# Optimization experiments

Hardware: AMD Instinct MI355X
Metric: run time of the kernel (lower is better)

The kernel has to match this reference:

```python
import jax, jax.numpy as jnp
import numpy as np

COV_LOSS_WT = 1.0


def setup_inputs() -> dict:
    key = jax.random.key(0)
    ks = jax.random.split(key, 6)
    B, T, S, H = 8, 64, 256, 768
    sc = 1.0 / np.sqrt(H)
    return {
        "decoder_outputs": jax.random.normal(ks[0], (B, T, H), jnp.float32),
        "decoder_input_mask": jnp.ones((B, T), jnp.float32),
        "encoder_outputs": jax.random.normal(ks[1], (B, S, H), jnp.float32),
        "enc_padding_mask": jnp.ones((B, S), jnp.float32),
        "coverage": jnp.zeros((B, S), jnp.float32),
        "W_h": (jax.random.normal(ks[2], (H, H), jnp.float32) * sc),
        "W_dec": (jax.random.normal(ks[3], (H, H), jnp.float32) * sc),
        "b_dec": jnp.zeros((H,), jnp.float32),
        "w_c": (jax.random.normal(ks[4], (H,), jnp.float32) * sc),
        "v": (jax.random.normal(ks[5], (H,), jnp.float32) * sc),
    }


def reference(decoder_outputs, decoder_input_mask, encoder_outputs,
              enc_padding_mask, coverage, W_h, W_dec, b_dec, w_c, v):
    # Precompute projections (same math as expanding att_features then adding
    # the coverage feature per step).
    enc_feature = encoder_outputs @ W_h.T                 # [B,S,H]
    dec_fea = decoder_outputs @ W_dec.T + b_dec           # [B,T,H]

    def step(cov, dec_t):
        # cov: [B,S], dec_t: [B,H]
        e = jnp.tanh(enc_feature + dec_t[:, None, :] + cov[:, :, None] * w_c)  # [B,S,H]
        scores = e @ v                                    # [B,S]
        attn = jax.nn.softmax(scores, axis=-1) * enc_padding_mask
        attn = attn / attn.sum(-1, keepdims=True)
        ht = jnp.einsum('bs,bsh->bh', attn, encoder_outputs)
        step_loss = COV_LOSS_WT * jnp.sum(jnp.minimum(attn, cov), axis=-1)     # [B]
        return cov + attn, (ht, attn, step_loss)

    coverage_final, (ht, attn, step_losses) = jax.lax.scan(
        step, coverage, jnp.swapaxes(dec_fea, 0, 1))      # scan over T

    ht_hat = jnp.swapaxes(ht, 0, 1)                       # [B,T,H]
    attn_dist = jnp.swapaxes(attn, 0, 1)                  # [B,T,S]
    converge_loss = jnp.sum(step_losses * decoder_input_mask.T) / jnp.sum(decoder_input_mask)
    return (ht_hat, attn_dist, converge_loss, coverage_final)
```

## Files before the change

### kernel.cpp

```cpp
#include <hip/hip_runtime.h>

#define Bq 8
#define Tq 64
#define Sq 256
#define Hq 768
#define TT 8
#define ST 16

typedef float f32x4 __attribute__((ext_vector_type(4)));
typedef __bf16 bf16x8 __attribute__((ext_vector_type(8)));

#define TANH_SCALE 2.885390081777927f
#define LOG2E 1.4426950408889634f

template <int Ctrl, int Rmask>
__device__ __forceinline__ float dpp_add_f(float v) {
  int t = __builtin_amdgcn_update_dpp(0, __float_as_int(v), Ctrl, Rmask, 0xF, true);
  return v + __int_as_float(t);
}
__device__ __forceinline__ float wave64_sum(float v) {
  v = dpp_add_f<0xB1, 0xF>(v);
  v = dpp_add_f<0x4E, 0xF>(v);
  v = dpp_add_f<0x141, 0xF>(v);
  v = dpp_add_f<0x140, 0xF>(v);
  v = dpp_add_f<0x142, 0xA>(v);
  v = dpp_add_f<0x143, 0xC>(v);
  return __int_as_float(__builtin_amdgcn_readlane(__float_as_int(v), 63));
}

__device__ __forceinline__ uint2 cvt4(f32x4 v) {
  union { __bf16 h[4]; uint2 u; } t;
  t.h[0] = (__bf16)v[0]; t.h[1] = (__bf16)v[1];
  t.h[2] = (__bf16)v[2]; t.h[3] = (__bf16)v[3];
  return t.u;
}

__global__ __launch_bounds__(256, 4) void proj_kernel(
    const float* __restrict__ enc, const float* __restrict__ dec,
    const float* __restrict__ Wh, const float* __restrict__ Wd,
    const float* __restrict__ bd,
    const float* __restrict__ wcvec, const float* __restrict__ vvec,
    __bf16* __restrict__ efh, __bf16* __restrict__ decfh,
    float* __restrict__ w1g, float* __restrict__ lacc)
{
  {
    int gidx = blockIdx.x * 256 + threadIdx.x;
    if (gidx < Hq) w1g[gidx] = vvec[gidx] * wcvec[gidx];
    if (gidx == 0) lacc[0] = 0.f;
  }

  __shared__ unsigned short As[2][32][40];
  __shared__ unsigned short Bs[2][64][40];

  int bid = blockIdx.x;
  const float* A; const float* W; bool isEf;
  int bm, bn;
  if (bid < 768) {
    A = enc; W = Wh; isEf = true;
    bm = bid % 64; bn = bid / 64;
  } else {
    bid -= 768;
    A = dec; W = Wd; isEf = false;
    bm = bid % 16; bn = bid / 16;
  }
  const int m0 = bm * 32, n0 = bn * 64;

  const int ti = threadIdx.x;
  const int rowA = ti >> 3, colA = (ti & 7) * 4;
  const int rowB = ti >> 2, colB = (ti & 3) * 8;
  const float* pa = A + (size_t)(m0 + rowA) * Hq + colA;
  const float* pw = W + (size_t)(n0 + rowB) * Hq + colB;

  {
    f32x4 a0 = *(const f32x4*)pa;
    f32x4 w0 = *(const f32x4*)pw, w1 = *(const f32x4*)(pw + 4);
    *(uint2*)&As[0][rowA][colA]     = cvt4(a0);
    *(uint2*)&Bs[0][rowB][colB]     = cvt4(w0);
    *(uint2*)&Bs[0][rowB][colB + 4] = cvt4(w1);
  }
  __syncthreads();

  const int w = ti >> 6, ln = ti & 63;
  const int mh = (w >> 1) * 16, nh = (w & 1) * 32;
  const int rsel = ln & 15, kofe = (ln >> 4) * 8;

  f32x4 acc[2] = {};
  for (int k = 0; k < 24; k++) {
    f32x4 na, nw0, nw1;
    if (k < 23) {
      na  = *(const f32x4*)(pa + (k + 1) * 32);
      nw0 = *(const f32x4*)(pw + (k + 1) * 32);
      nw1 = *(const f32x4*)(pw + (k + 1) * 32 + 4);
    }
    const int cur = k & 1;
    bf16x8 af = *(const bf16x8*)&As[cur][mh + rsel][kofe];
    bf16x8 b0 = *(const bf16x8*)&Bs[cur][nh + rsel][kofe];
    bf16x8 b1 = *(const bf16x8*)&Bs[cur][nh + 16 + rsel][kofe];
    acc[0] = __builtin_amdgcn_mfma_f32_16x16x32_bf16(af, b0, acc[0], 0, 0, 0);
    acc[1] = __builtin_amdgcn_mfma_f32_16x16x32_bf16(af, b1, acc[1], 0, 0, 0);
    if (k < 23) {
      const int nxt = cur ^ 1;
      *(uint2*)&As[nxt][rowA][colA]     = cvt4(na);
      *(uint2*)&Bs[nxt][rowB][colB]     = cvt4(nw0);
      *(uint2*)&Bs[nxt][rowB][colB + 4] = cvt4(nw1);
      __syncthreads();
    }
  }

  const int col = ln & 15, rb = (ln >> 4) * 4;
#pragma unroll
  for (int tn = 0; tn < 2; tn++)
#pragma unroll
    for (int j = 0; j < 4; j++) {
      int r = m0 + mh + rb + j, c = n0 + nh + tn * 16 + col;
      float val = acc[tn][j];
      if (isEf) {
        efh[(size_t)r * Hq + c] =
            (__bf16)__builtin_amdgcn_exp2f(val * TANH_SCALE);
      } else {
        decfh[(size_t)r * Hq + c] =
            (__bf16)__builtin_amdgcn_exp2f((val + bd[c]) * TANH_SCALE);
      }
    }
}

__global__ __launch_bounds__(256, 4) void abcd_kernel(
    const __bf16* __restrict__ efh, const __bf16* __restrict__ decfh,
    const float* __restrict__ vvec, const float* __restrict__ w1g,
    float2* __restrict__ ab)
{
  __shared__ unsigned short efs[ST][780];
  __shared__ unsigned short dts[TT][776];
  __shared__ float part[128][2];
  const int b = blockIdx.x & 7;
  const int r = blockIdx.x >> 3;
  const int tt0 = (r & 7) * TT;
  const int st0 = (r >> 3) * ST;
  const int tid = threadIdx.x;

  for (int i = tid; i < ST * 192; i += 256) {
    int row = i / 192, c = (i % 192) * 4;
    *(uint2*)&efs[row][c] =
        *(const uint2*)(efh + (size_t)(b * Sq + st0 + row) * Hq + c);
  }
  for (int i = tid; i < TT * 192; i += 256) {
    int row = i / 192, c = (i % 192) * 4;
    *(uint2*)&dts[row][c] =
        *(const uint2*)(decfh + (size_t)(b * Tq + tt0 + row) * Hq + c);
  }
  __syncthreads();

  const int hh = tid >> 7;
  const int pid = tid & 127;
  const int tl = pid >> 4, sl = pid & 15;
  const int hbase = hh * 384;
  const int hbu = __builtin_amdgcn_readfirstlane(hbase);
  const float* vp  = vvec + hbu;
  const float* w1p = w1g + hbu;

  float A = 0.f, B = 0.f;
#define BLO(x) __uint_as_float((x) << 16)
#define BHI(x) __uint_as_float((x) & 0xFFFF0000u)
#pragma unroll 4
  for (int j = 0; j < 384; j += 4) {
    uint2 eu = *(const uint2*)&efs[sl][hbase + j];
    uint2 du = *(const uint2*)&dts[tl][hbase + j];
    f32x4 v4 = *(const f32x4*)(vp + j);
    f32x4 w1 = *(const f32x4*)(w1p + j);
    float e2[4];
    e2[0] = BLO(eu.x) * BLO(du.x);
    e2[1] = BHI(eu.x) * BHI(du.x);
    e2[2] = BLO(eu.y) * BLO(du.y);
    e2[3] = BHI(eu.y) * BHI(du.y);
#pragma unroll
    for (int e = 0; e < 4; e++) {
      float rr = __builtin_amdgcn_rcpf(1.f + e2[e]);
      float t0 = 1.f - 2.f * rr;
      float f1 = 1.f - t0 * t0;
      A += v4[e] * t0;
      B += w1[e] * f1;
    }
  }
#undef BLO
#undef BHI

  if (hh == 1) { part[pid][0] = A; part[pid][1] = B; }
  __syncthreads();
  if (hh == 0) {
    float2 outv;
    outv.x = A + part[pid][0];
    outv.y = B + part[pid][1];
    ab[(size_t)(b * Tq + tt0 + tl) * Sq + st0 + sl] = outv;
  }
}

__global__ __launch_bounds__(256, 1) void scan2_kernel(
    const float2* __restrict__ ab, const float* __restrict__ emask,
    const float* __restrict__ cov0, const float* __restrict__ dmask,
    float* __restrict__ out_attn, float* __restrict__ out_covf,
    float* __restrict__ lacc)
{
  __shared__ float zp[2][4];
  __shared__ float dms[Tq];
  __shared__ float lred[4];
  const int b = blockIdx.x;
  const int s = threadIdx.x;
  const int w = s >> 6, ln = s & 63;
  if (s < Tq) dms[s] = dmask[b * Tq + s];
  const float em = emask[b * Sq + s];
  float cov = cov0[b * Sq + s];
  float lp = 0.f;
  const float2* P = ab + (size_t)b * Tq * Sq + s;
  float2 cur = P[0];
  __syncthreads();

  for (int t = 0; t < Tq; t++) {
    float2 nxt = (t + 1 < Tq) ? P[(size_t)(t + 1) * Sq] : cur;
    float sc = cur.x + cov * cur.y;
    float E = __builtin_amdgcn_exp2f(sc * LOG2E) * em;
    float wsum = wave64_sum(E);
    if (ln == 0) zp[t & 1][w] = wsum;
    __syncthreads();
    float Z = zp[t & 1][0] + zp[t & 1][1] + zp[t & 1][2] + zp[t & 1][3];
    float at = E * __builtin_amdgcn_rcpf(Z);
    lp += fminf(at, cov) * dms[t];
    cov += at;
    out_attn[(size_t)(b * Tq + t) * Sq + s] = at;
    cur = nxt;
  }

  out_covf[b * Sq + s] = cov;
  float wl = wave64_sum(lp);
  if (ln == 0) lred[w] = wl;
  __syncthreads();
  if (s == 0) atomicAdd(lacc, lred[0] + lred[1] + lred[2] + lred[3]);
}

__global__ __launch_bounds__(256) void ht_kernel(
    const float* __restrict__ attn, const float* __restrict__ enc,
    const float* __restrict__ dmask, const float* __restrict__ lacc,
    float* __restrict__ out_ht, float* __restrict__ out_loss)
{
  __shared__ float lat[Sq][8];
  __shared__ float r4[4];
  int bid = blockIdx.x;
  int b = bid / 24, r = bid % 24, tc = r / 3, hc = r % 3;
  int tid = threadIdx.x;
  int h = hc * 256 + tid;
#pragma unroll
  for (int tt = 0; tt < 8; tt++)
    lat[tid][tt] = attn[(size_t)(b * Tq + tc * 8 + tt) * Sq + tid];
  __syncthreads();

  float acc[8] = {};
  const float* ep = enc + (size_t)(b * Sq) * Hq + h;
  for (int sb = 0; sb < Sq; sb += 8) {
    float e[8];
#pragma unroll
    for (int u = 0; u < 8; u++) e[u] = ep[(size_t)(sb + u) * Hq];
#pragma unroll
    for (int u = 0; u < 8; u++) {
      f32x4 a0 = *(const f32x4*)&lat[sb + u][0];
      f32x4 a1 = *(const f32x4*)&lat[sb + u][4];
      acc[0] += a0[0] * e[u]; acc[1] += a0[1] * e[u];
      acc[2] += a0[2] * e[u]; acc[3] += a0[3] * e[u];
      acc[4] += a1[0] * e[u]; acc[5] += a1[1] * e[u];
      acc[6] += a1[2] * e[u]; acc[7] += a1[3] * e[u];
    }
  }
#pragma unroll
  for (int tt = 0; tt < 8; tt++)
    out_ht[(size_t)(b * Tq + tc * 8 + tt) * Hq + h] = acc[tt];

  if (blockIdx.x == 0) {
    float s = 0.f;
    for (int i = tid; i < Bq * Tq; i += 256) s += dmask[i];
#pragma unroll
    for (int off = 32; off; off >>= 1) s += __shfl_xor(s, off);
    int w = tid >> 6, ln = tid & 63;
    if (ln == 0) r4[w] = s;
    __syncthreads();
    if (tid == 0) out_loss[0] = lacc[0] / (r4[0] + r4[1] + r4[2] + r4[3]);
  }
}

extern "C" void kernel_launch(void* const* d_in, const int* in_sizes, int n_in,
                              void* d_out, int out_size, void* d_ws, size_t ws_size,
                              hipStream_t stream) {
  const float* dec   = (const float*)d_in[0];
  const float* dmask = (const float*)d_in[1];
  const float* enc   = (const float*)d_in[2];
  const float* emask = (const float*)d_in[3];
  const float* cov0  = (const float*)d_in[4];
  const float* Wh    = (const float*)d_in[5];
  const float* Wd    = (const float*)d_in[6];
  const float* bd    = (const float*)d_in[7];
  const float* wc    = (const float*)d_in[8];
  const float* vv    = (const float*)d_in[9];
  float* out = (float*)d_out;

  char* ws = (char*)d_ws;
  __bf16* efh   = (__bf16*)ws;
  __bf16* decfh = (__bf16*)(ws + 3145728);
  float2* ab    = (float2*)(ws + 3932160);
  float*  w1g   = (float*)(ws + 4980736);
  float*  lacc  = (float*)(ws + 4983808);

  const size_t OFF_ATTN = (size_t)Bq * Tq * Hq;
  const size_t OFF_LOSS = OFF_ATTN + (size_t)Bq * Tq * Sq;
  const size_t OFF_COV  = OFF_LOSS + 1;

  proj_kernel<<<960, 256, 0, stream>>>(enc, dec, Wh, Wd, bd, wc, vv,
                                       efh, decfh, w1g, lacc);
  abcd_kernel<<<1024, 256, 0, stream>>>(efh, decfh, vv, w1g, ab);
  scan2_kernel<<<Bq, 256, 0, stream>>>(ab, emask, cov0, dmask,
                                       out + OFF_ATTN, out + OFF_COV, lacc);
  ht_kernel<<<192, 256, 0, stream>>>(out + OFF_ATTN, enc, dmask, lacc,
                                     out, out + OFF_LOSS);
}
```

Baseline: 90.92 us.

## Fuse score computation and coverage scan with per-chunk counters for overlap

Merges the score-producing kernel and the sequential softmax/coverage scan into one launch. The 8 scan blocks take the highest block indices and spin on per-(batch, time-chunk) atomic counters, so they can start on early time chunks while the remaining score blocks are still running. This removes a kernel launch boundary and overlaps the serial scan with producer work. The risk is deadlock or slowdown if the scan blocks get scheduled before producers, since the scan blocks occupy CUs while polling. It also relies on relaxed atomics with no acquire/release ordering between the ab stores and the counter.

```diff
diff --git a/kernel.cpp b/kernel.cpp
--- a/kernel.cpp
+++ b/kernel.cpp
@@ -41,11 +41,13 @@
     const float* __restrict__ bd,
     const float* __restrict__ wcvec, const float* __restrict__ vvec,
     __bf16* __restrict__ efh, __bf16* __restrict__ decfh,
-    float* __restrict__ w1g, float* __restrict__ lacc)
+    float* __restrict__ w1g, float* __restrict__ lacc,
+    unsigned* __restrict__ cnt)
 {
   {
     int gidx = blockIdx.x * 256 + threadIdx.x;
     if (gidx < Hq) w1g[gidx] = vvec[gidx] * wcvec[gidx];
+    if (gidx < 64) cnt[gidx] = 0u;
     if (gidx == 0) lacc[0] = 0.f;
   }
 
@@ -124,116 +126,138 @@
     }
 }
 
-__global__ __launch_bounds__(256, 4) void abcd_kernel(
+__global__ __launch_bounds__(256, 4) void abscan_kernel(
     const __bf16* __restrict__ efh, const __bf16* __restrict__ decfh,
     const float* __restrict__ vvec, const float* __restrict__ w1g,
-    float2* __restrict__ ab)
+    const float* __restrict__ emask, const float* __restrict__ cov0,
+    const float* __restrict__ dmask,
+    float2* __restrict__ ab,
+    float* __restrict__ out_attn, float* __restrict__ out_covf,
+    float* __restrict__ lacc, unsigned* __restrict__ cnt)
 {
-  __shared__ unsigned short efs[ST][780];
-  __shared__ unsigned short dts[TT][776];
-  __shared__ float part[128][2];
-  const int b = blockIdx.x & 7;
-  const int r = blockIdx.x >> 3;
-  const int tt0 = (r & 7) * TT;
-  const int st0 = (r >> 3) * ST;
+  __shared__ double smem_raw[4808];
+  const int bid = blockIdx.x;
   const int tid = threadIdx.x;
 
-  for (int i = tid; i < ST * 192; i += 256) {
-    int row = i / 192, c = (i % 192) * 4;
-    *(uint2*)&efs[row][c] =
-        *(const uint2*)(efh + (size_t)(b * Sq + st0 + row) * Hq + c);
-  }
-  for (int i = tid; i < TT * 192; i += 256) {
-    int row = i / 192, c = (i % 192) * 4;
-    *(uint2*)&dts[row][c] =
-        *(const uint2*)(decfh + (size_t)(b * Tq + tt0 + row) * Hq + c);
-  }
-  __syncthreads();
-
-  const int hh = tid >> 7;
-  const int pid = tid & 127;
-  const int tl = pid >> 4, sl = pid & 15;
-  const int hbase = hh * 384;
-  const int hbu = __builtin_amdgcn_readfirstlane(hbase);
-  const float* vp  = vvec + hbu;
-  const float* w1p = w1g + hbu;
-
-  float A = 0.f, B = 0.f;
+  if (bid < 1024) {
+    unsigned short (*efs)[780] = (unsigned short(*)[780])smem_raw;
+    unsigned short (*dts)[776] = (unsigned short(*)[776])((char*)smem_raw + 24960);
+    float (*part)[2]           = (float(*)[2])((char*)smem_raw + 37376);
+    const int b = bid & 7;
+    const int r = bid >> 3;
+    const int kchunk = r & 7;
+    const int tt0 = kchunk * TT;
+    const int st0 = (r >> 3) * ST;
+
+    for (int i = tid; i < ST * 192; i += 256) {
+      int row = i / 192, c = (i % 192) * 4;
+      *(uint2*)&efs[row][c] =
+          *(const uint2*)(efh + (size_t)(b * Sq + st0 + row) * Hq + c);
+    }
+    for (int i = tid; i < TT * 192; i += 256) {
+      int row = i / 192, c = (i % 192) * 4;
+      *(uint2*)&dts[row][c] =
+          *(const uint2*)(decfh + (size_t)(b * Tq + tt0 + row) * Hq + c);
+    }
+    __syncthreads();
+
+    const int hh = tid >> 7;
+    const int pid = tid & 127;
+    const int tl = pid >> 4, sl = pid & 15;
+    const int hbase = hh * 384;
+    const int hbu = __builtin_amdgcn_readfirstlane(hbase);
+    const float* vp  = vvec + hbu;
+    const float* w1p = w1g + hbu;
+
+    float A = 0.f, B = 0.f;
 #define BLO(x) __uint_as_float((x) << 16)
 #define BHI(x) __uint_as_float((x) & 0xFFFF0000u)
 #pragma unroll 4
-  for (int j = 0; j < 384; j += 4) {
-    uint2 eu = *(const uint2*)&efs[sl][hbase + j];
-    uint2 du = *(const uint2*)&dts[tl][hbase + j];
-    f32x4 v4 = *(const f32x4*)(vp + j);
-    f32x4 w1 = *(const f32x4*)(w1p + j);
-    float e2[4];
-    e2[0] = BLO(eu.x) * BLO(du.x);
-    e2[1] = BHI(eu.x) * BHI(du.x);
-    e2[2] = BLO(eu.y) * BLO(du.y);
-    e2[3] = BHI(eu.y) * BHI(du.y);
-#pragma unroll
-    for (int e = 0; e < 4; e++) {
-      float rr = __builtin_amdgcn_rcpf(1.f + e2[e]);
-      float t0 = 1.f - 2.f * rr;
-      float f1 = 1.f - t0 * t0;
-      A += v4[e] * t0;
-      B += w1[e] * f1;
-    }
-  }
+    for (int j = 0; j < 384; j += 4) {
+      uint2 eu = *(const uint2*)&efs[sl][hbase + j];
+      uint2 du = *(const uint2*)&dts[tl][hbase + j];
+      f32x4 v4 = *(const f32x4*)(vp + j);
+      f32x4 w1 = *(const f32x4*)(w1p + j);
+      float e2[4];
+      e2[0] = BLO(eu.x) * BLO(du.x);
+      e2[1] = BHI(eu.x) * BHI(du.x);
+      e2[2] = BLO(eu.y) * BLO(du.y);
+      e2[3] = BHI(eu.y) * BHI(du.y);
+#pragma unroll
+      for (int e = 0; e < 4; e++) {
+        float rr = __builtin_amdgcn_rcpf(1.f + e2[e]);
+        float t0 = 1.f - 2.f * rr;
+        float f1 = 1.f - t0 * t0;
+        A += v4[e] * t0;
+        B += w1[e] * f1;
+      }
+    }
 #undef BLO
 #undef BHI
 
-  if (hh == 1) { part[pid][0] = A; part[pid][1] = B; }
-  __syncthreads();
-  if (hh == 0) {
-    float2 outv;
-    outv.x = A + part[pid][0];
-    outv.y = B + part[pid][1];
-    ab[(size_t)(b * Tq + tt0 + tl) * Sq + st0 + sl] = outv;
-  }
-}
-
-__global__ __launch_bounds__(256, 1) void scan2_kernel(
-    const float2* __restrict__ ab, const float* __restrict__ emask,
-    const float* __restrict__ cov0, const float* __restrict__ dmask,
-    float* __restrict__ out_attn, float* __restrict__ out_covf,
-    float* __restrict__ lacc)
-{
-  __shared__ float zp[2][4];
-  __shared__ float dms[Tq];
-  __shared__ float lred[4];
-  const int b = blockIdx.x;
-  const int s = threadIdx.x;
-  const int w = s >> 6, ln = s & 63;
-  if (s < Tq) dms[s] = dmask[b * Tq + s];
-  const float em = emask[b * Sq + s];
-  float cov = cov0[b * Sq + s];
-  float lp = 0.f;
-  const float2* P = ab + (size_t)b * Tq * Sq + s;
-  float2 cur = P[0];
-  __syncthreads();
-
-  for (int t = 0; t < Tq; t++) {
-    float2 nxt = (t + 1 < Tq) ? P[(size_t)(t + 1) * Sq] : cur;
-    float sc = cur.x + cov * cur.y;
-    float E = __builtin_amdgcn_exp2f(sc * LOG2E) * em;
-    float wsum = wave64_sum(E);
-    if (ln == 0) zp[t & 1][w] = wsum;
-    __syncthreads();
-    float Z = zp[t & 1][0] + zp[t & 1][1] + zp[t & 1][2] + zp[t & 1][3];
-    float at = E * __builtin_amdgcn_rcpf(Z);
-    lp += fminf(at, cov) * dms[t];
-    cov += at;
-    out_attn[(size_t)(b * Tq + t) * Sq + s] = at;
-    cur = nxt;
-  }
-
-  out_covf[b * Sq + s] = cov;
-  float wl = wave64_sum(lp);
-  if (ln == 0) lred[w] = wl;
-  __syncthreads();
-  if (s == 0) atomicAdd(lacc, lred[0] + lred[1] + lred[2] + lred[3]);
+    if (hh == 1) { part[pid][0] = A; part[pid][1] = B; }
+    __syncthreads();
+    if (hh == 0) {
+      union { float2 f; unsigned long long u; } cv;
+      cv.f.x = A + part[pid][0];
+      cv.f.y = B + part[pid][1];
+      __hip_atomic_store(
+          (unsigned long long*)&ab[(size_t)(b * Tq + tt0 + tl) * Sq + st0 + sl],
+          cv.u, __ATOMIC_RELAXED, __HIP_MEMORY_SCOPE_AGENT);
+    }
+    __syncthreads();
+    if (tid == 0)
+      __hip_atomic_fetch_add(&cnt[b * 8 + kchunk], 1u,
+                             __ATOMIC_RELAXED, __HIP_MEMORY_SCOPE_AGENT);
+  } else {
+    float* zp   = (float*)smem_raw;
+    float* dms  = (float*)smem_raw + 8;
+    float* lred = (float*)smem_raw + 72;
+    const int b = bid - 1024;
+    const int s = tid, w = tid >> 6, ln = tid & 63;
+    if (tid < Tq) dms[tid] = dmask[b * Tq + tid];
+    const float em = emask[b * Sq + s];
+    float cov = cov0[b * Sq + s];
+    float lp = 0.f;
+    const unsigned long long* P =
+        (const unsigned long long*)(ab + (size_t)b * Tq * Sq + s);
+
+    for (int kc = 0; kc < 8; kc++) {
+      if (tid == 0)
+        while (__hip_atomic_load(&cnt[b * 8 + kc],
+                                 __ATOMIC_RELAXED, __HIP_MEMORY_SCOPE_AGENT) < 16u)
+          __builtin_amdgcn_s_sleep(2);
+      __syncthreads();
+
+      union { unsigned long long u; float2 f; } cv[8];
+#pragma unroll
+      for (int j = 0; j < 8; j++)
+        cv[j].u = __hip_atomic_load(P + (size_t)(kc * 8 + j) * Sq,
+                                    __ATOMIC_RELAXED, __HIP_MEMORY_SCOPE_AGENT);
+
+#pragma unroll
+      for (int j = 0; j < 8; j++) {
+        const int t = kc * 8 + j;
+        float sc = cv[j].f.x + cov * cv[j].f.y;
+        float E = __builtin_amdgcn_exp2f(sc * LOG2E) * em;
+        float wsum = wave64_sum(E);
+        if (ln == 0) zp[(t & 1) * 4 + w] = wsum;
+        __syncthreads();
+        float Z = zp[(t & 1) * 4 + 0] + zp[(t & 1) * 4 + 1] +
+                  zp[(t & 1) * 4 + 2] + zp[(t & 1) * 4 + 3];
+        float at = E * __builtin_amdgcn_rcpf(Z);
+        lp += fminf(at, cov) * dms[t];
+        cov += at;
+        out_attn[(size_t)(b * Tq + t) * Sq + s] = at;
+      }
+    }
+
+    out_covf[b * Sq + s] = cov;
+    float wl = wave64_sum(lp);
+    if (ln == 0) lred[w] = wl;
+    __syncthreads();
+    if (tid == 0) atomicAdd(lacc, lred[0] + lred[1] + lred[2] + lred[3]);
+  }
 }
 
 __global__ __launch_bounds__(256) void ht_kernel(
@@ -300,21 +324,23 @@
   float* out = (float*)d_out;
 
   char* ws = (char*)d_ws;
-  __bf16* efh   = (__bf16*)ws;
-  __bf16* decfh = (__bf16*)(ws + 3145728);
-  float2* ab    = (float2*)(ws + 3932160);
-  float*  w1g   = (float*)(ws + 4980736);
-  float*  lacc  = (float*)(ws + 4983808);
+  __bf16*   efh   = (__bf16*)ws;
+  __bf16*   decfh = (__bf16*)(ws + 3145728);
+  float2*   ab    = (float2*)(ws + 3932160);
+  float*    w1g   = (float*)(ws + 4980736);
+  float*    lacc  = (float*)(ws + 4983808);
+  unsigned* cnt   = (unsigned*)(ws + 4983872);
 
   const size_t OFF_ATTN = (size_t)Bq * Tq * Hq;
   const size_t OFF_LOSS = OFF_ATTN + (size_t)Bq * Tq * Sq;
   const size_t OFF_COV  = OFF_LOSS + 1;
 
   proj_kernel<<<960, 256, 0, stream>>>(enc, dec, Wh, Wd, bd, wc, vv,
-                                       efh, decfh, w1g, lacc);
-  abcd_kernel<<<1024, 256, 0, stream>>>(efh, decfh, vv, w1g, ab);
-  scan2_kernel<<<Bq, 256, 0, stream>>>(ab, emask, cov0, dmask,
-                                       out + OFF_ATTN, out + OFF_COV, lacc);
+                                       efh, decfh, w1g, lacc, cnt);
+  abscan_kernel<<<1032, 256, 0, stream>>>(efh, decfh, vv, w1g, emask, cov0,
+                                          dmask, ab,
+                                          out + OFF_ATTN, out + OFF_COV,
+                                          lacc, cnt);
   ht_kernel<<<192, 256, 0, stream>>>(out + OFF_ATTN, enc, dmask, lacc,
                                      out, out + OFF_LOSS);
 }
```

Result: faster. 84.94 us (-6.6%).
